# Kernel tuning notes

Measured on AMD Instinct MI355X. Metric: run time of the kernel, lower is better.

The kernel has to match this reference:

```python
import jax, jax.numpy as jnp
import numpy as np
from math import sqrt

B, S, E, H = 2, 2048, 768, 12
DH = E // H
W = 256            # one-sided attention window (attention_window=512)
G = 16             # number of global tokens (positions 0..G-1 in every batch row)
PAD = 128          # last PAD tokens per row are padding (masked)
FF = 3072          # SwiGLU intermediate size
NEG = -1e9
EPS = 1e-5


def _ln(x, g, b):
    m = jnp.mean(x, axis=-1, keepdims=True)
    v = jnp.var(x, axis=-1, keepdims=True)
    return (x - m) * jax.lax.rsqrt(v + EPS) * g + b


def _rope(x, t):
    # x: [B,H,S,DH]; t: [B,S] float 'set positions'
    half = DH // 2
    inv_freq = 1.0 / (10000.0 ** (jnp.arange(half, dtype=jnp.float32) / half))
    ang = t[:, None, :, None] * inv_freq            # [B,1,S,half]
    cos, sin = jnp.cos(ang), jnp.sin(ang)
    x1, x2 = x[..., :half], x[..., half:]
    return jnp.concatenate([x1 * cos - x2 * sin, x2 * cos + x1 * sin], axis=-1)


def _heads(x):  # [B,S,E] -> [B,H,S,DH]
    return x.reshape(B, S, H, DH).transpose(0, 2, 1, 3)


def _chunk3(x):
    # [B,H,S,D] -> [B,H,C,3W,D]: for query chunk c, keys from chunks c-1,c,c+1 (zero padded)
    b, h, s, d = x.shape
    c = s // W
    xp = jnp.pad(x, ((0, 0), (0, 0), (W, W), (0, 0))).reshape(b, h, c + 2, W, d)
    return jnp.concatenate([xp[:, :, :-2], xp[:, :, 1:-1], xp[:, :, 2:]], axis=3)


def _forward(x, attention_mask, global_attention_mask,
             Wq, bq, Wk, bk, Wv, bv, Wqg, bqg, Wkg, bkg, Wvg, bvg,
             ln0_g, ln0_b, ln1_g, ln1_b, W1, W3, W2):
    C = S // W
    merged = attention_mask * (global_attention_mask + 1)   # 0 masked, 1 local, 2 global
    is_masked = merged == 0
    is_global = merged == 2
    remove = merged != 1   # keys removed from windowed attention (masked or global)

    q = _heads(x @ Wq + bq) / sqrt(DH)
    k = _heads(x @ Wk + bk)
    v = _heads(x @ Wv + bv)

    # RoPE over 'set positions': (~is_index_masked) * cumsum(is_index_global_attn)
    t = jnp.where(is_masked, 0, jnp.cumsum(is_global.astype(jnp.int32), axis=1)).astype(jnp.float32)
    q = _rope(q, t)
    k = _rope(k, t)

    # --- sliding-window (banded) scores: band[b,h,i,d] = q_i . k_{i+d-W} ---
    qc = q.reshape(B, H, C, W, DH)
    k3 = _chunk3(k)
    s3 = jnp.einsum('bhcpd,bhcqd->bhcpq', qc, k3)                     # [B,H,C,W,3W]
    didx = jnp.arange(W)[:, None] + jnp.arange(2 * W + 1)[None, :]    # [W,2W+1]
    band = jnp.take_along_axis(s3, didx[None, None, None], axis=-1)   # [B,H,C,W,2W+1]

    # mask removed keys / out-of-range positions inside the band
    rmp = jnp.pad(remove, ((0, 0), (W, W)), constant_values=True).reshape(B, C + 2, W)
    rm3 = jnp.concatenate([rmp[:, :-2], rmp[:, 1:-1], rmp[:, 2:]], axis=2)  # [B,C,3W]
    band_rm = jnp.take_along_axis(jnp.broadcast_to(rm3[:, :, None, :], (B, C, W, 3 * W)),
                                  didx[None, None], axis=-1)                # [B,C,W,2W+1]
    band = jnp.where(band_rm[:, None], NEG, band).reshape(B, H, S, 2 * W + 1)

    # --- global-key columns (keys taken from the RoPE'd local key vectors) ---
    sg = jnp.einsum('bhid,bhgd->bhig', q, k[:, :, :G])                # [B,H,S,G]

    scores = jnp.concatenate([sg, band], axis=-1)                     # [B,H,S,G+2W+1]
    probs = jax.nn.softmax(scores.astype(jnp.float32), axis=-1).astype(x.dtype)
    probs = jnp.where(is_masked[:, None, :, None], 0.0, probs)

    # --- probs @ value: global columns + band ---
    out = jnp.einsum('bhig,bhgd->bhid', probs[..., :G], v[:, :, :G])
    pl = probs[..., G:].reshape(B, H, C, W, 2 * W + 1)
    rows = jnp.broadcast_to(jnp.arange(W)[:, None], (W, 2 * W + 1))
    p3 = jnp.zeros((B, H, C, W, 3 * W), probs.dtype).at[:, :, :, rows, didx].set(pl)
    v3 = _chunk3(v)
    out = out + jnp.einsum('bhcpq,bhcqd->bhcpd', p3, v3).reshape(B, H, S, DH)
    attn = out.transpose(0, 2, 1, 3).reshape(B, S, E)

    # --- full attention for global tokens (separate global projections, no RoPE) ---
    gq = _heads(x @ Wqg + bqg)[:, :, :G] / sqrt(DH)                   # [B,H,G,DH]
    gk = _heads(x @ Wkg + bkg)
    gv = _heads(x @ Wvg + bvg)
    gs = jnp.einsum('bhgd,bhjd->bhgj', gq, gk)                        # [B,H,G,S]
    gs = jnp.where(is_masked[:, None, None, :], NEG, gs)
    gp = jax.nn.softmax(gs.astype(jnp.float32), axis=-1).astype(x.dtype)
    gout = jnp.einsum('bhgj,bhjd->bhgd', gp, gv).transpose(0, 2, 1, 3).reshape(B, G, E)
    attn = attn.at[:, :G].set(gout)

    # residual + post-LN, SwiGLU FFN, residual + post-LN (dropout = eval mode)
    h0 = _ln(x + attn, ln0_g, ln0_b)
    ffn = (jax.nn.silu(h0 @ W1) * (h0 @ W3)) @ W2
    return _ln(h0 + ffn, ln1_g, ln1_b)


def setup_inputs():
    key = jax.random.key(0)
    ks = jax.random.split(key, 12)
    x = jax.random.normal(ks[0], (B, S, E), jnp.float32)
    attention_mask = jnp.ones((B, S), jnp.int32).at[:, S - PAD:].set(0)
    global_attention_mask = jnp.zeros((B, S), jnp.int32).at[:, :G].set(1)
    sd = 0.02
    def w(k, shape):
        return jax.random.normal(k, shape, jnp.float32) * sd
    return dict(
        x=x, attention_mask=attention_mask, global_attention_mask=global_attention_mask,
        Wq=w(ks[1], (E, E)), bq=jnp.zeros((E,), jnp.float32),
        Wk=w(ks[2], (E, E)), bk=jnp.zeros((E,), jnp.float32),
        Wv=w(ks[3], (E, E)), bv=jnp.zeros((E,), jnp.float32),
        Wqg=w(ks[4], (E, E)), bqg=jnp.zeros((E,), jnp.float32),
        Wkg=w(ks[5], (E, E)), bkg=jnp.zeros((E,), jnp.float32),
        Wvg=w(ks[6], (E, E)), bvg=jnp.zeros((E,), jnp.float32),
        ln0_g=jnp.ones((E,), jnp.float32), ln0_b=jnp.zeros((E,), jnp.float32),
        ln1_g=jnp.ones((E,), jnp.float32), ln1_b=jnp.zeros((E,), jnp.float32),
        W1=w(ks[7], (E, FF)), W3=w(ks[8], (E, FF)), W2=w(ks[9], (FF, E)))


def reference(x, attention_mask, global_attention_mask, Wq, bq, Wk, bk, Wv, bv,
              Wqg, bqg, Wkg, bkg, Wvg, bvg, ln0_g, ln0_b, ln1_g, ln1_b, W1, W3, W2):
    return _forward(x, attention_mask, global_attention_mask,
                    Wq, bq, Wk, bk, Wv, bv, Wqg, bqg, Wkg, bkg, Wvg, bvg,
                    ln0_g, ln0_b, ln1_g, ln1_b, W1, W3, W2)
```

## Files before the change

### kernel.cpp

```cpp
#include <hip/hip_runtime.h>


#define BB_ 2
#define SS 2048
#define EE 768
#define HH 12
#define DHH 64
#define GG 16
#define FFN 3072
#define MM (BB_*SS)

typedef __bf16 bf16_t;
typedef __bf16 bf16x8_t __attribute__((ext_vector_type(8)));
typedef float f32x4_t __attribute__((ext_vector_type(4)));

__device__ inline void gload16(const void* g, void* l) {
  __builtin_amdgcn_global_load_lds((const __attribute__((address_space(1))) void*)g,
                                   (__attribute__((address_space(3))) void*)l, 16, 0, 0);
}

__global__ __launch_bounds__(64) void detect_kernel(const unsigned int* __restrict__ w,
                                                    int* __restrict__ flag) {
  int cnt = 0;
  for (int i = threadIdx.x; i < 1024; i += 64) {
    unsigned e = (w[i] >> 7) & 0xFF;
    cnt += (e >= 100 && e <= 144) ? 1 : 0;
  }
  for (int off = 32; off; off >>= 1) cnt += __shfl_xor(cnt, off);
  if (threadIdx.x == 0) flag[0] = (cnt > 512) ? 1 : 0;
}

struct CanonP { const void* src[11]; bf16_t* dst[11]; };

__global__ __launch_bounds__(256) void canon_kernel(CanonP P, const int* __restrict__ flag) {
  constexpr int ns[11] = {3145728, 768,768,768,768,768,768, 768,768,768,768};
  int idx4 = (blockIdx.x*256 + threadIdx.x)*4;
  const bool isb = flag[0] != 0;
  int off = 0, seg = -1, loc = 0;
  #pragma unroll
  for (int i=0;i<11;i++) {
    if (seg < 0 && idx4 < off + ns[i]) { seg = i; loc = idx4 - off; }
    off += ns[i];
  }
  if (seg < 0) return;
  const void* s = P.src[seg];
  bf16_t* d = P.dst[seg];
  if (isb) {
    *(uint2*)&d[loc] = *(const uint2*)((const unsigned short*)s + loc);
  } else {
    float4 v = *(const float4*)((const float*)s + loc);
    d[loc+0] = (bf16_t)v.x; d[loc+1] = (bf16_t)v.y;
    d[loc+2] = (bf16_t)v.z; d[loc+3] = (bf16_t)v.w;
  }
}

struct TP6 { const void* s[6]; bf16_t* d[6]; };

__global__ __launch_bounds__(256) void trans_kernel(TP6 P, int R, int C,
                                                    const int* __restrict__ flag) {
  const int z = blockIdx.z;
  const void* src = P.s[z]; bf16_t* dst = P.d[z];
  const bool isb = flag[0] != 0;
  __shared__ bf16_t tile[32][33];
  int tx = threadIdx.x & 31, ty = threadIdx.x >> 5;
  int r0 = blockIdx.y*32, c0 = blockIdx.x*32;
  #pragma unroll
  for (int i=0;i<4;i++) {
    int rr = ty + i*8;
    size_t si = (size_t)(r0+rr)*C + c0 + tx;
    tile[rr][tx] = isb ? ((const bf16_t*)src)[si] : (bf16_t)((const float*)src)[si];
  }
  __syncthreads();
  #pragma unroll
  for (int i=0;i<4;i++) {
    int cc = ty + i*8;
    dst[(size_t)(c0+cc)*R + r0 + tx] = tile[tx][cc];
  }
}

__global__ __launch_bounds__(256) void zero_kernel(float* __restrict__ p, int n) {
  int i = blockIdx.x*256 + threadIdx.x;
  if (i < n) p[i] = 0.f;
}

__global__ __launch_bounds__(256) void flags_kernel(const int* __restrict__ am,
                                                    const int* __restrict__ gm,
                                                    float* __restrict__ tpos,
                                                    int* __restrict__ flags) {
  int b = blockIdx.x;
  int t = threadIdx.x;
  int lane = t & 63, wv = t >> 6;
  int base = b*SS + t*8;
  int mg[8]; int isg[8]; int loc = 0;
  for (int i=0;i<8;i++) {
    int a = am[base+i], g = gm[base+i];
    int merged = a*(g+1);
    mg[i] = merged;
    isg[i] = (merged==2) ? 1 : 0;
    loc += isg[i];
  }
  int x = loc;
  for (int off=1; off<64; off<<=1) {
    int y = __shfl_up(x, off);
    if (lane >= off) x += y;
  }
  __shared__ int wtot[4];
  if (lane==63) wtot[wv] = x;
  __syncthreads();
  int prev = 0;
  for (int w=0; w<wv; w++) prev += wtot[w];
  int run = prev + x - loc;
  for (int i=0;i<8;i++) {
    run += isg[i];
    int masked = (mg[i]==0) ? 1 : 0;
    int glob   = (mg[i]==2) ? 1 : 0;
    int rem    = (mg[i]!=1) ? 1 : 0;
    tpos[base+i]  = masked ? 0.f : (float)run;
    flags[base+i] = masked | (glob<<1) | (rem<<2);
  }
}

__device__ inline void gemm128_core(const bf16_t* __restrict__ A,
                                    const bf16_t* __restrict__ BT,
                                    int ldA, int ldB, int kbeg, int kend,
                                    int m0, int n0,
                                    bf16_t* As, bf16_t* Bs,
                                    f32x4_t (&acc)[4][4]) {
  const int t = threadIdx.x;
  const int lane = t & 63, wv = t >> 6;
  const int l15 = lane & 15, quad = lane >> 4;
  const int wr = (wv >> 1) << 6, wc = (wv & 1) << 6;
  const int rsub = lane >> 3, pch = lane & 7;
  const int sch = pch ^ rsub;
  const size_t abase = (size_t)(m0 + wv*32 + rsub)*ldA + sch*8;
  const size_t bbase = (size_t)(n0 + wv*32 + rsub)*ldB + sch*8;
  const int sx = l15 & 7;
  bf16_t* lA = As + (wv*32)*64;
  bf16_t* lB = Bs + (wv*32)*64;
  for (int k0 = kbeg; k0 < kend; k0 += 64) {
    __syncthreads();
    #pragma unroll
    for (int j=0;j<4;j++) {
      gload16(A + abase + (size_t)(j*8)*ldA + k0, lA + j*8*64);
      gload16(BT + bbase + (size_t)(j*8)*ldB + k0, lB + j*8*64);
    }
    __syncthreads();
    #pragma unroll
    for (int c=0;c<2;c++) {
      bf16x8_t af[4], bfr[4];
      #pragma unroll
      for (int a=0;a<4;a++)
        af[a] = *(const bf16x8_t*)&As[(wr + a*16 + l15)*64 + ((c*4+quad)^sx)*8];
      #pragma unroll
      for (int b=0;b<4;b++)
        bfr[b] = *(const bf16x8_t*)&Bs[(wc + b*16 + l15)*64 + ((c*4+quad)^sx)*8];
      #pragma unroll
      for (int a=0;a<4;a++)
        #pragma unroll
        for (int b=0;b<4;b++)
          acc[a][b] = __builtin_amdgcn_mfma_f32_16x16x32_bf16(af[a], bfr[b], acc[a][b], 0,0,0);
    }
  }
}

struct ProjParams {
  const bf16_t* W[5];
  const bf16_t* Bi[5];
  bf16_t* O[5];
};

__global__ __launch_bounds__(256) void proj_kernel(const bf16_t* __restrict__ x,
                                                   ProjParams P,
                                                   const float* __restrict__ tpos) {
  const int m0 = blockIdx.x*128, n0 = blockIdx.y*128;
  const int z  = blockIdx.z;
  __shared__ bf16_t As[128*64];
  __shared__ bf16_t Bs[128*64];
  f32x4_t acc[4][4];
  #pragma unroll
  for (int a=0;a<4;a++)
    #pragma unroll
    for (int b=0;b<4;b++) acc[a][b] = (f32x4_t){0.f,0.f,0.f,0.f};
  gemm128_core(x, P.W[z], EE, EE, 0, EE, m0, n0, As, Bs, acc);

  const int t = threadIdx.x;
  const int lane = t & 63, wv = t >> 6;
  const int l15 = lane & 15, quad = lane >> 4;
  const int wr = (wv >> 1) << 6, wc = (wv & 1) << 6;
  const float scale = (z==0) ? 0.125f : 1.f;
  const bool rope = (z<2);
  const int h = (n0 + wc) >> 6;
  bf16_t* Oz = P.O[z];
  const bf16_t* Bz = P.Bi[z];
  float bvals[4];
  #pragma unroll
  for (int b=0;b<4;b++) bvals[b] = (float)Bz[h*64 + b*16 + l15];
  #pragma unroll
  for (int a=0;a<4;a++) {
    #pragma unroll
    for (int r=0;r<4;r++) {
      int row = m0 + wr + a*16 + quad*4 + r;
      int bb = row >> 11, spos = row & (SS-1);
      float vals[4];
      #pragma unroll
      for (int b=0;b<4;b++) vals[b] = (acc[a][b][r] + bvals[b]) * scale;
      if (rope) {
        float tv = tpos[row];
        #pragma unroll
        for (int b=0;b<2;b++) {
          int j = b*16 + l15;
          float inv = __expf(-(float)j * (9.210340371976184f/32.f));
          float ang = tv * inv;
          float sn = __sinf(ang), cs = __cosf(ang);
          float x1 = vals[b], x2 = vals[b+2];
          vals[b]   = x1*cs - x2*sn;
          vals[b+2] = x2*cs + x1*sn;
        }
      }
      bf16_t* dst = Oz + ((size_t)(bb*HH + h)*SS + spos)*DHH;
      #pragma unroll
      for (int b=0;b<4;b++) dst[b*16 + l15] = (bf16_t)vals[b];
    }
  }
}

__global__ __launch_bounds__(256) void gemm_ffn1(const bf16_t* __restrict__ A,
                                                 const bf16_t* __restrict__ BT,
                                                 bf16_t* __restrict__ t1) {
  const int m0 = blockIdx.x*128, n0 = blockIdx.y*128;
  __shared__ bf16_t As[128*64];
  __shared__ bf16_t Bs[128*64];
  f32x4_t acc[4][4];
  #pragma unroll
  for (int a=0;a<4;a++)
    #pragma unroll
    for (int b=0;b<4;b++) acc[a][b] = (f32x4_t){0.f,0.f,0.f,0.f};
  gemm128_core(A, BT, EE, EE, 0, EE, m0, n0, As, Bs, acc);
  const int t = threadIdx.x;
  const int lane = t & 63, wv = t >> 6;
  const int l15 = lane & 15, quad = lane >> 4;
  const int wr = (wv >> 1) << 6, wc = (wv & 1) << 6;
  #pragma unroll
  for (int a=0;a<4;a++)
    #pragma unroll
    for (int r=0;r<4;r++) {
      int row = m0 + wr + a*16 + quad*4 + r;
      #pragma unroll
      for (int b=0;b<4;b++)
        t1[(size_t)row*FFN + n0 + wc + b*16 + l15] = (bf16_t)acc[a][b][r];
    }
}

__global__ __launch_bounds__(256) void gemm_ffn3(const bf16_t* __restrict__ A,
                                                 const bf16_t* __restrict__ BT,
                                                 const bf16_t* __restrict__ t1,
                                                 bf16_t* __restrict__ g1) {
  const int m0 = blockIdx.x*128, n0 = blockIdx.y*128;
  __shared__ bf16_t As[128*64];
  __shared__ bf16_t Bs[128*64];
  f32x4_t acc[4][4];
  #pragma unroll
  for (int a=0;a<4;a++)
    #pragma unroll
    for (int b=0;b<4;b++) acc[a][b] = (f32x4_t){0.f,0.f,0.f,0.f};
  gemm128_core(A, BT, EE, EE, 0, EE, m0, n0, As, Bs, acc);
  const int t = threadIdx.x;
  const int lane = t & 63, wv = t >> 6;
  const int l15 = lane & 15, quad = lane >> 4;
  const int wr = (wv >> 1) << 6, wc = (wv & 1) << 6;
  #pragma unroll
  for (int a=0;a<4;a++)
    #pragma unroll
    for (int r=0;r<4;r++) {
      int row = m0 + wr + a*16 + quad*4 + r;
      #pragma unroll
      for (int b=0;b<4;b++) {
        size_t idx = (size_t)row*FFN + n0 + wc + b*16 + l15;
        float a1 = (float)t1[idx];
        float sil = a1 / (1.f + __expf(-a1));
        g1[idx] = (bf16_t)(sil * acc[a][b][r]);
      }
    }
}

struct Ffn2Out { float* p[4]; };

__global__ __launch_bounds__(256) void gemm_ffn2(const bf16_t* __restrict__ A,
                                                 const bf16_t* __restrict__ BT,
                                                 Ffn2Out O) {
  const int m0 = blockIdx.x*128, n0 = blockIdx.y*128;
  const int kz = blockIdx.z;
  __shared__ bf16_t As[128*64];
  __shared__ bf16_t Bs[128*64];
  f32x4_t acc[4][4];
  #pragma unroll
  for (int a=0;a<4;a++)
    #pragma unroll
    for (int b=0;b<4;b++) acc[a][b] = (f32x4_t){0.f,0.f,0.f,0.f};
  gemm128_core(A, BT, FFN, FFN, kz*768, (kz+1)*768, m0, n0, As, Bs, acc);
  const int t = threadIdx.x;
  const int lane = t & 63, wv = t >> 6;
  const int l15 = lane & 15, quad = lane >> 4;
  const int wr = (wv >> 1) << 6, wc = (wv & 1) << 6;
  float* C = O.p[kz];
  #pragma unroll
  for (int a=0;a<4;a++)
    #pragma unroll
    for (int r=0;r<4;r++) {
      int row = m0 + wr + a*16 + quad*4 + r;
      #pragma unroll
      for (int b=0;b<4;b++)
        C[(size_t)row*EE + n0 + wc + b*16 + l15] = acc[a][b][r];
    }
}

__global__ __launch_bounds__(64) void qg_kernel(const bf16_t* __restrict__ x,
                                                const bf16_t* __restrict__ WqgT,
                                                const bf16_t* __restrict__ bqg,
                                                float* __restrict__ qgb) {
  int g = blockIdx.x, h = blockIdx.y, b = blockIdx.z;
  int d = threadIdx.x;
  __shared__ float xs[EE];
  for (int i=d; i<EE; i+=64) xs[i] = (float)x[((size_t)b*SS + g)*EE + i];
  __syncthreads();
  float acc = 0.f;
  const bf16_t* wrow = WqgT + (size_t)(h*64+d)*EE;
  #pragma unroll 4
  for (int k=0;k<EE;k+=8) {
    bf16x8_t w8 = *(const bf16x8_t*)(wrow + k);
    #pragma unroll
    for (int i=0;i<8;i++) acc += xs[k+i] * (float)w8[i];
  }
  acc = (acc + (float)bqg[h*64+d]) * 0.125f;
  qgb[((size_t)(b*HH+h)*GG + g)*DHH + d] = acc;
}

__global__ __launch_bounds__(256) void band_kernel(const bf16_t* __restrict__ qb,
                                                   const bf16_t* __restrict__ kb,
                                                   const bf16_t* __restrict__ vb,
                                                   const int* __restrict__ flags,
                                                   float* __restrict__ attn) {
  const int p0 = blockIdx.x*64;
  const int h = blockIdx.y, b = blockIdx.z;
  const int t = threadIdx.x;
  const int wv = t>>6, lane = t&63;
  const int l15 = lane & 15, quad = lane >> 4;
  const size_t bh = (size_t)(b*HH+h);
  const bf16_t* kbh = kb + bh*SS*DHH;
  const bf16_t* vbh = vb + bh*SS*DHH;
  const int* fl = flags + b*SS;
  const int q0 = p0 + wv*16;

  __shared__ bf16_t Vt[64*72];
  __shared__ bf16_t Pw[4][16*72];

  const bf16_t* qrow = qb + (bh*SS + q0 + l15)*DHH;
  bf16x8_t qa0 = *(const bf16x8_t*)(qrow + quad*8);
  bf16x8_t qa1 = *(const bf16x8_t*)(qrow + 32 + quad*8);

  f32x4_t o[4];
  #pragma unroll
  for (int i=0;i<4;i++) o[i] = (f32x4_t){0.f,0.f,0.f,0.f};
  float lsum[4] = {0.f,0.f,0.f,0.f};
  bf16_t* P = Pw[wv];

  for (int unit=0; unit<10; unit++) {
    const int kb0 = (unit<9) ? (p0 - 256 + unit*64) : 0;
    __syncthreads();
    {
      int kp  = (t & 31)*2;
      int dh0 = (t >> 5)*8;
      int k1 = kb0 + kp, k2 = kb0 + kp + 1;
      int kc1 = min(max(k1,0),SS-1), kc2 = min(max(k2,0),SS-1);
      bf16x8_t v1 = *(const bf16x8_t*)(vbh + (size_t)kc1*DHH + dh0);
      bf16x8_t v2 = *(const bf16x8_t*)(vbh + (size_t)kc2*DHH + dh0);
      #pragma unroll
      for (int i=0;i<8;i++) {
        union { unsigned u; bf16_t hh[2]; } pk;
        pk.hh[0] = v1[i]; pk.hh[1] = v2[i];
        *(unsigned*)&Vt[(dh0+i)*72 + kp] = pk.u;
      }
    }
    __syncthreads();
    const int nsub = (unit<9) ? 4 : 1;
    for (int sub=0; sub<4; sub++) {
      if (sub < nsub) {
        int kpos = kb0 + sub*16 + l15;
        int kc = min(max(kpos,0),SS-1);
        const bf16_t* krow = kbh + (size_t)kc*DHH;
        bf16x8_t kf0 = *(const bf16x8_t*)(krow + quad*8);
        bf16x8_t kf1 = *(const bf16x8_t*)(krow + 32 + quad*8);
        f32x4_t s = (f32x4_t){0.f,0.f,0.f,0.f};
        s = __builtin_amdgcn_mfma_f32_16x16x32_bf16(qa0, kf0, s, 0,0,0);
        s = __builtin_amdgcn_mfma_f32_16x16x32_bf16(qa1, kf1, s, 0,0,0);
        bool drop = false;
        if (unit<9) drop = (kpos<0) || (kpos>=SS) || (((fl[kc]>>2)&1)!=0);
        #pragma unroll
        for (int r=0;r<4;r++) {
          float e;
          if (unit==9) {
            e = __expf(s[r]);
          } else {
            int dj = kpos - (q0 + quad*4 + r);
            bool valid = (dj>=-256) && (dj<=256) && (!drop);
            e = valid ? __expf(s[r]) : 0.f;
          }
          lsum[r] += e;
          P[(quad*4+r)*72 + sub*16 + l15] = (bf16_t)e;
        }
      } else {
        #pragma unroll
        for (int r=0;r<4;r++) P[(quad*4+r)*72 + sub*16 + l15] = (bf16_t)0.f;
      }
    }
    #pragma unroll
    for (int chunk=0; chunk<2; chunk++) {
      bf16x8_t pf = *(const bf16x8_t*)&P[l15*72 + chunk*32 + quad*8];
      #pragma unroll
      for (int nt=0; nt<4; nt++) {
        bf16x8_t vf = *(const bf16x8_t*)&Vt[(nt*16+l15)*72 + chunk*32 + quad*8];
        o[nt] = __builtin_amdgcn_mfma_f32_16x16x32_bf16(pf, vf, o[nt], 0,0,0);
      }
    }
  }
  #pragma unroll
  for (int r=0;r<4;r++) {
    float s = lsum[r];
    s += __shfl_xor(s,1); s += __shfl_xor(s,2);
    s += __shfl_xor(s,4); s += __shfl_xor(s,8);
    lsum[r] = s;
  }
  #pragma unroll
  for (int r=0;r<4;r++) {
    int q = q0 + quad*4 + r;
    int masked = fl[q] & 1;
    float inv = masked ? 0.f : 1.f/lsum[r];
    float* dst = attn + ((size_t)(b*SS+q))*EE + h*64 + l15;
    #pragma unroll
    for (int nt=0; nt<4; nt++) dst[nt*16] = o[nt][r]*inv;
  }
}

__global__ __launch_bounds__(256) void gattn_part(const float* __restrict__ qgb,
                                                  const bf16_t* __restrict__ kgb,
                                                  const bf16_t* __restrict__ vgb,
                                                  const int* __restrict__ flags,
                                                  float* __restrict__ go,
                                                  float* __restrict__ gl) {
  const int kbase = blockIdx.x*128;
  const int h = blockIdx.y, b = blockIdx.z;
  const int t = threadIdx.x;
  __shared__ float gqs[16*68];
  __shared__ float Ks[64*68];
  __shared__ float Vs[64*68];
  __shared__ float es[16*64];
  const size_t bh = (size_t)(b*HH+h);
  #pragma unroll
  for (int j=0;j<4;j++) {
    int idx = t + j*256;
    int g = idx>>6, d = idx&63;
    gqs[g*68+d] = qgb[(bh*GG + g)*DHH + d];
  }
  float accv[4] = {0.f,0.f,0.f,0.f};
  float lpart = 0.f;
  const int gs = t>>4, kslot = t&15;
  const int dp = t&63, grp = t>>6;
  const bf16_t* kb_ = kgb + bh*SS*DHH;
  const bf16_t* vb_ = vgb + bh*SS*DHH;
  const int* fl = flags + b*SS;
  for (int tile=0; tile<2; tile++) {
    int k0 = kbase + tile*64;
    __syncthreads();
    {
      int row = t>>2, seg = t&3;
      const bf16_t* sk = kb_ + (size_t)(k0+row)*DHH + seg*16;
      const bf16_t* sv = vb_ + (size_t)(k0+row)*DHH + seg*16;
      bf16x8_t k1 = *(const bf16x8_t*)sk;
      bf16x8_t k2 = *(const bf16x8_t*)(sk+8);
      bf16x8_t v1 = *(const bf16x8_t*)sv;
      bf16x8_t v2 = *(const bf16x8_t*)(sv+8);
      #pragma unroll
      for (int i=0;i<8;i++) {
        Ks[row*68 + seg*16 + i]     = (float)k1[i];
        Ks[row*68 + seg*16 + 8 + i] = (float)k2[i];
        Vs[row*68 + seg*16 + i]     = (float)v1[i];
        Vs[row*68 + seg*16 + 8 + i] = (float)v2[i];
      }
    }
    __syncthreads();
    #pragma unroll
    for (int j=0;j<4;j++) {
      int key = kslot + 16*j;
      const float* gq = &gqs[gs*68];
      const float* kr = &Ks[key*68];
      float s = 0.f;
      #pragma unroll
      for (int d4=0; d4<64; d4+=4) {
        float4 a = *(const float4*)(gq + d4);
        float4 kk = *(const float4*)(kr + d4);
        s += a.x*kk.x + a.y*kk.y + a.z*kk.z + a.w*kk.w;
      }
      int msk = fl[k0+key] & 1;
      float e = msk ? 0.f : __expf(s);
      es[gs*64+key] = e;
      lpart += e;
    }
    __syncthreads();
    #pragma unroll
    for (int g=0; g<4; g++) {
      int gg = grp*4+g;
      float a = accv[g];
      for (int key=0;key<64;key++) a += es[gg*64+key]*Vs[key*68+dp];
      accv[g] = a;
    }
  }
  __syncthreads();
  es[gs*64 + kslot] = lpart;
  __syncthreads();
  if (t < 16) {
    float s = 0.f;
    for (int j=0;j<16;j++) s += es[t*64+j];
    atomicAdd(&gl[bh*16 + t], s);
  }
  #pragma unroll
  for (int g=0; g<4; g++)
    atomicAdd(&go[(bh*16 + grp*4+g)*64 + dp], accv[g]);
}

__global__ __launch_bounds__(256) void addln_kernel(const bf16_t* __restrict__ Abf,
                                                    const float* __restrict__ Af,
                                                    const float* __restrict__ B0,
                                                    const float* __restrict__ B1,
                                                    const float* __restrict__ B2,
                                                    const float* __restrict__ B3,
                                                    const float* __restrict__ gof,
                                                    const float* __restrict__ glf,
                                                    const bf16_t* __restrict__ gw,
                                                    const bf16_t* __restrict__ bw,
                                                    float* __restrict__ outf,
                                                    bf16_t* __restrict__ outb,
                                                    const int* __restrict__ flagp) {
  int r = blockIdx.x, t = threadIdx.x;
  int lane = t&63, wv = t>>6;
  int spos = r & (SS-1), bb = r >> 11;
  bool isglob = (gof != nullptr) && (spos < GG);
  float v[3]; float sum=0.f, ss=0.f;
  #pragma unroll
  for (int j=0;j<3;j++) {
    int idx = t + j*256;
    size_t gi = (size_t)r*EE+idx;
    float a = Abf ? (float)Abf[gi] : Af[gi];
    float bv;
    if (isglob) {
      int hh = idx >> 6, dp = idx & 63;
      int slot = (bb*HH + hh)*GG + spos;
      bv = gof[(size_t)slot*DHH + dp] / glf[slot];
    } else {
      bv = B0[gi];
    }
    float val = a + bv;
    if (B1) val += B1[gi] + B2[gi] + B3[gi];
    v[j] = val; sum += val; ss += val*val;
  }
  #pragma unroll
  for (int off=32; off>=1; off>>=1) {
    sum += __shfl_xor(sum, off);
    ss  += __shfl_xor(ss, off);
  }
  __shared__ float s1[4], s2[4];
  if (lane==0) { s1[wv]=sum; s2[wv]=ss; }
  __syncthreads();
  sum = s1[0]+s1[1]+s1[2]+s1[3];
  ss  = s2[0]+s2[1]+s2[2]+s2[3];
  float mean = sum * (1.f/(float)EE);
  float var  = ss * (1.f/(float)EE) - mean*mean;
  float rstd = rsqrtf(var + 1e-5f);
  bool wantb, wantf;
  if (flagp) { bool isb = (*flagp)!=0; wantb = isb; wantf = !isb; }
  else { wantb = (outb!=nullptr); wantf = (outf!=nullptr); }
  #pragma unroll
  for (int j=0;j<3;j++) {
    int idx = t + j*256;
    float o = (v[j]-mean)*rstd*(float)gw[idx] + (float)bw[idx];
    if (wantf) outf[(size_t)r*EE+idx] = o;
    if (wantb) outb[(size_t)r*EE+idx] = (bf16_t)o;
  }
}

extern "C" void kernel_launch(void* const* d_in, const int* in_sizes, int n_in,
                              void* d_out, int out_size, void* d_ws, size_t ws_size,
                              hipStream_t stream) {
  const void* x_r    = d_in[0];
  const int* am      = (const int*)d_in[1];
  const int* gm      = (const int*)d_in[2];
  (void)in_sizes; (void)n_in; (void)out_size; (void)ws_size;

  char* ws = (char*)d_ws;
  size_t off = 0;
  auto alloc = [&](size_t bytes) -> void* {
    void* p = ws + off;
    off += (bytes + 255) & ~(size_t)255;
    return p;
  };
  bf16_t* xc    = (bf16_t*)alloc((size_t)MM*EE*2);
  bf16_t* WT[6]; bf16_t* bc[6];
  for (int i=0;i<6;i++) { WT[i] = (bf16_t*)alloc((size_t)EE*EE*2); bc[i] = (bf16_t*)alloc(EE*2); }
  bf16_t* lnc[4];
  for (int i=0;i<4;i++) lnc[i] = (bf16_t*)alloc(EE*2);
  bf16_t* W1T = (bf16_t*)alloc((size_t)EE*FFN*2);
  bf16_t* W3T = (bf16_t*)alloc((size_t)EE*FFN*2);
  bf16_t* W2T = (bf16_t*)alloc((size_t)FFN*EE*2);
  const size_t NBHSD = (size_t)BB_*HH*SS*DHH;
  bf16_t* qb    = (bf16_t*)alloc(NBHSD*2);
  bf16_t* kb    = (bf16_t*)alloc(NBHSD*2);
  bf16_t* vb    = (bf16_t*)alloc(NBHSD*2);
  bf16_t* kgb   = (bf16_t*)alloc(NBHSD*2);
  bf16_t* vgb   = (bf16_t*)alloc(NBHSD*2);
  float* qgb   = (float*)alloc((size_t)BB_*HH*GG*DHH*4);
  float* attn  = (float*)alloc((size_t)MM*EE*4);
  float* h0f   = (float*)alloc((size_t)MM*EE*4);
  bf16_t* h0b  = (bf16_t*)alloc((size_t)MM*EE*2);
  bf16_t* g1   = (bf16_t*)alloc((size_t)MM*FFN*2);
  float* p3    = (float*)alloc((size_t)MM*EE*4);
  float* go    = (float*)alloc((size_t)BB_*HH*GG*DHH*4);
  float* gl    = (float*)alloc((size_t)BB_*HH*GG*4);
  float* tposb = (float*)alloc((size_t)BB_*SS*4);
  int*   flagb = (int*)alloc((size_t)BB_*SS*4);
  int*   dflag = (int*)alloc(256);
  bf16_t* t1 = qb;
  float* p1 = (float*)qb;
  float* p2 = (float*)qb + (size_t)MM*EE;

  detect_kernel<<<1, 64, 0, stream>>>((const unsigned int*)d_in[3], dflag);

  CanonP CP;
  const void* csrc[11] = { x_r, d_in[4], d_in[6], d_in[8], d_in[10], d_in[12], d_in[14],
                           d_in[15], d_in[16], d_in[17], d_in[18] };
  bf16_t* cdst[11] = { xc, bc[0], bc[1], bc[2], bc[3], bc[4], bc[5],
                       lnc[0], lnc[1], lnc[2], lnc[3] };
  for (int i=0;i<11;i++) { CP.src[i]=csrc[i]; CP.dst[i]=cdst[i]; }
  canon_kernel<<<3081, 256, 0, stream>>>(CP, dflag);

  TP6 T6;
  const int wi[6] = {3,5,7,9,11,13};
  for (int i=0;i<6;i++) { T6.s[i]=d_in[wi[i]]; T6.d[i]=WT[i]; }
  trans_kernel<<<dim3(24,24,6), 256, 0, stream>>>(T6, EE, EE, dflag);
  TP6 TF; TF.s[0]=d_in[19]; TF.d[0]=W1T; TF.s[1]=d_in[20]; TF.d[1]=W3T;
  for (int i=2;i<6;i++) { TF.s[i]=d_in[19]; TF.d[i]=W1T; }
  trans_kernel<<<dim3(96,24,2), 256, 0, stream>>>(TF, EE, FFN, dflag);
  TP6 T2; T2.s[0]=d_in[21]; T2.d[0]=W2T;
  for (int i=1;i<6;i++) { T2.s[i]=d_in[21]; T2.d[i]=W2T; }
  trans_kernel<<<dim3(24,96,1), 256, 0, stream>>>(T2, FFN, EE, dflag);

  zero_kernel<<<98, 256, 0, stream>>>(go, 24960);

  flags_kernel<<<BB_, 256, 0, stream>>>(am, gm, tposb, flagb);

  ProjParams P;
  P.W[0]=WT[0]; P.Bi[0]=bc[0]; P.O[0]=qb;
  P.W[1]=WT[1]; P.Bi[1]=bc[1]; P.O[1]=kb;
  P.W[2]=WT[2]; P.Bi[2]=bc[2]; P.O[2]=vb;
  P.W[3]=WT[4]; P.Bi[3]=bc[4]; P.O[3]=kgb;
  P.W[4]=WT[5]; P.Bi[4]=bc[5]; P.O[4]=vgb;
  proj_kernel<<<dim3(MM/128, EE/128, 5), 256, 0, stream>>>(xc, P, tposb);

  qg_kernel<<<dim3(GG, HH, BB_), 64, 0, stream>>>(xc, WT[3], bc[3], qgb);

  band_kernel<<<dim3(SS/64, HH, BB_), 256, 0, stream>>>(qb, kb, vb, flagb, attn);

  gattn_part<<<dim3(SS/128, HH, BB_), 256, 0, stream>>>(qgb, kgb, vgb, flagb, go, gl);

  addln_kernel<<<MM, 256, 0, stream>>>(xc, nullptr, attn, nullptr, nullptr, nullptr,
                                       go, gl, lnc[0], lnc[1], h0f, h0b, nullptr);

  gemm_ffn1<<<dim3(MM/128, FFN/128), 256, 0, stream>>>(h0b, W1T, t1);
  gemm_ffn3<<<dim3(MM/128, FFN/128), 256, 0, stream>>>(h0b, W3T, t1, g1);
  Ffn2Out FO; FO.p[0]=attn; FO.p[1]=p1; FO.p[2]=p2; FO.p[3]=p3;
  gemm_ffn2<<<dim3(MM/128, EE/128, 4), 256, 0, stream>>>(g1, W2T, FO);

  addln_kernel<<<MM, 256, 0, stream>>>(nullptr, h0f, attn, p1, p2, p3,
                                       nullptr, nullptr, lnc[2], lnc[3],
                                       (float*)d_out, (bf16_t*)d_out, dflag);
}
```

Baseline: 392.3 us.

## Double-buffer V tile in band attention and prefetch K fragments per unit

The band attention kernel now double-buffers the transposed V tile in shared memory. It loads the next unit's V rows into registers while the current unit computes, and writes them to the other buffer afterward, which removes one barrier per iteration. All four K fragments for a unit are loaded up front so the global loads overlap. The block index is also swizzled so neighbouring blocks process non-adjacent query chunks. The cost is more registers and shared memory per block, which may lower occupancy.

```diff
diff --git a/kernel.cpp b/kernel.cpp
--- a/kernel.cpp
+++ b/kernel.cpp
@@ -340,7 +340,8 @@
                                                    const bf16_t* __restrict__ vb,
                                                    const int* __restrict__ flags,
                                                    float* __restrict__ attn) {
-  const int p0 = blockIdx.x*64;
+  const int bswz = (int)((blockIdx.x & 7)*4 + (blockIdx.x >> 3));
+  const int p0 = bswz*64;
   const int h = blockIdx.y, b = blockIdx.z;
   const int t = threadIdx.x;
   const int wv = t>>6, lane = t&63;
@@ -351,48 +352,63 @@
   const int* fl = flags + b*SS;
   const int q0 = p0 + wv*16;
 
-  __shared__ bf16_t Vt[64*72];
+  __shared__ bf16_t Vt[2][64*72];
   __shared__ bf16_t Pw[4][16*72];
 
   const bf16_t* qrow = qb + (bh*SS + q0 + l15)*DHH;
   bf16x8_t qa0 = *(const bf16x8_t*)(qrow + quad*8);
   bf16x8_t qa1 = *(const bf16x8_t*)(qrow + 32 + quad*8);
 
+  const int kpV = (t & 31)*2;
+  const int dhV = (t >> 5)*8;
+
   f32x4_t o[4];
   #pragma unroll
   for (int i=0;i<4;i++) o[i] = (f32x4_t){0.f,0.f,0.f,0.f};
   float lsum[4] = {0.f,0.f,0.f,0.f};
   bf16_t* P = Pw[wv];
 
+  bf16x8_t vA, vB;
+  {
+    int k1 = min(max(p0-256+kpV,0),SS-1), k2 = min(max(p0-256+kpV+1,0),SS-1);
+    vA = *(const bf16x8_t*)(vbh + (size_t)k1*DHH + dhV);
+    vB = *(const bf16x8_t*)(vbh + (size_t)k2*DHH + dhV);
+    #pragma unroll
+    for (int i=0;i<8;i++) {
+      union { unsigned u; bf16_t hh[2]; } pk;
+      pk.hh[0] = vA[i]; pk.hh[1] = vB[i];
+      *(unsigned*)&Vt[0][(dhV+i)*72 + kpV] = pk.u;
+    }
+  }
+
   for (int unit=0; unit<10; unit++) {
+    const int cur = unit & 1;
     const int kb0 = (unit<9) ? (p0 - 256 + unit*64) : 0;
     __syncthreads();
-    {
-      int kp  = (t & 31)*2;
-      int dh0 = (t >> 5)*8;
-      int k1 = kb0 + kp, k2 = kb0 + kp + 1;
-      int kc1 = min(max(k1,0),SS-1), kc2 = min(max(k2,0),SS-1);
-      bf16x8_t v1 = *(const bf16x8_t*)(vbh + (size_t)kc1*DHH + dh0);
-      bf16x8_t v2 = *(const bf16x8_t*)(vbh + (size_t)kc2*DHH + dh0);
-      #pragma unroll
-      for (int i=0;i<8;i++) {
-        union { unsigned u; bf16_t hh[2]; } pk;
-        pk.hh[0] = v1[i]; pk.hh[1] = v2[i];
-        *(unsigned*)&Vt[(dh0+i)*72 + kp] = pk.u;
-      }
-    }
-    __syncthreads();
+    bf16x8_t kf[4][2];
+    #pragma unroll
+    for (int sub=0; sub<4; sub++) {
+      int kpos = kb0 + sub*16 + l15;
+      int kc = min(max(kpos,0),SS-1);
+      const bf16_t* krow = kbh + (size_t)kc*DHH;
+      kf[sub][0] = *(const bf16x8_t*)(krow + quad*8);
+      kf[sub][1] = *(const bf16x8_t*)(krow + 32 + quad*8);
+    }
+    if (unit < 9) {
+      int kbn = (unit<8) ? (kb0 + 64) : 0;
+      int k1 = min(max(kbn+kpV,0),SS-1), k2 = min(max(kbn+kpV+1,0),SS-1);
+      vA = *(const bf16x8_t*)(vbh + (size_t)k1*DHH + dhV);
+      vB = *(const bf16x8_t*)(vbh + (size_t)k2*DHH + dhV);
+    }
     const int nsub = (unit<9) ? 4 : 1;
+    #pragma unroll
     for (int sub=0; sub<4; sub++) {
       if (sub < nsub) {
         int kpos = kb0 + sub*16 + l15;
         int kc = min(max(kpos,0),SS-1);
-        const bf16_t* krow = kbh + (size_t)kc*DHH;
-        bf16x8_t kf0 = *(const bf16x8_t*)(krow + quad*8);
-        bf16x8_t kf1 = *(const bf16x8_t*)(krow + 32 + quad*8);
         f32x4_t s = (f32x4_t){0.f,0.f,0.f,0.f};
-        s = __builtin_amdgcn_mfma_f32_16x16x32_bf16(qa0, kf0, s, 0,0,0);
-        s = __builtin_amdgcn_mfma_f32_16x16x32_bf16(qa1, kf1, s, 0,0,0);
+        s = __builtin_amdgcn_mfma_f32_16x16x32_bf16(qa0, kf[sub][0], s, 0,0,0);
+        s = __builtin_amdgcn_mfma_f32_16x16x32_bf16(qa1, kf[sub][1], s, 0,0,0);
         bool drop = false;
         if (unit<9) drop = (kpos<0) || (kpos>=SS) || (((fl[kc]>>2)&1)!=0);
         #pragma unroll
@@ -418,8 +434,16 @@
       bf16x8_t pf = *(const bf16x8_t*)&P[l15*72 + chunk*32 + quad*8];
       #pragma unroll
       for (int nt=0; nt<4; nt++) {
-        bf16x8_t vf = *(const bf16x8_t*)&Vt[(nt*16+l15)*72 + chunk*32 + quad*8];
+        bf16x8_t vf = *(const bf16x8_t*)&Vt[cur][(nt*16+l15)*72 + chunk*32 + quad*8];
         o[nt] = __builtin_amdgcn_mfma_f32_16x16x32_bf16(pf, vf, o[nt], 0,0,0);
+      }
+    }
+    if (unit < 9) {
+      #pragma unroll
+      for (int i=0;i<8;i++) {
+        union { unsigned u; bf16_t hh[2]; } pk;
+        pk.hh[0] = vA[i]; pk.hh[1] = vB[i];
+        *(unsigned*)&Vt[cur^1][(dhV+i)*72 + kpV] = pk.u;
       }
     }
   }
```

Result: slower. 400.8 us (+2.2%).
